# Optimization experiments

Measured on AMD Instinct MI355X. Metric: run time of the kernel, lower is better.

Reference implementation:

```python
import jax, jax.numpy as jnp
import numpy as np

B, S = 8, 2048

def setup_inputs() -> dict:
    key = jax.random.key(0)
    ks = iter(jax.random.split(key, 64))
    def lin(din, dout):
        w = jax.random.normal(next(ks), (din, dout), jnp.float32) / np.float32(np.sqrt(din))
        b = jax.random.normal(next(ks), (dout,), jnp.float32) * 0.01
        return w, b
    inp = {}
    inp['x'] = jax.random.normal(next(ks), (B, S, 256), jnp.float32)
    def blk(tag, d, ff):
        for name, (din, dout) in [('q',(d,d)),('k',(d,d)),('v',(d,d)),('o',(d,d)),('ff1',(d,ff)),('ff2',(ff,d))]:
            w, b = lin(din, dout)
            inp[f'{name}_w{tag}'] = w; inp[f'{name}_b{tag}'] = b
        inp[f'ln1_g{tag}'] = jnp.ones((d,), jnp.float32); inp[f'ln1_b{tag}'] = jnp.zeros((d,), jnp.float32)
        inp[f'ln2_g{tag}'] = jnp.ones((d,), jnp.float32); inp[f'ln2_b{tag}'] = jnp.zeros((d,), jnp.float32)
    blk(1, 256, 1024)
    blk(2, 128, 512)
    for nm, (din, dout) in [('dr1',(256,128)),('dr2',(128,64)),('dr3',(64,32)),('dr4',(32,14))]:
        w, b = lin(din, dout)
        inp[f'{nm}_w'] = w; inp[f'{nm}_b'] = b
    return inp

def _ln(x, g, b, eps=1e-5):
    m = x.mean(-1, keepdims=True)
    v = ((x - m) ** 2).mean(-1, keepdims=True)
    return (x - m) / jnp.sqrt(v + eps) * g + b

def _mha(x, wq, bq, wk, bk, wv, bv, wo, bo, h):
    Bx, Sx, D = x.shape
    hd = D // h
    q = (x @ wq + bq).reshape(Bx, Sx, h, hd).transpose(0, 2, 1, 3)
    k = (x @ wk + bk).reshape(Bx, Sx, h, hd).transpose(0, 2, 1, 3)
    v = (x @ wv + bv).reshape(Bx, Sx, h, hd).transpose(0, 2, 1, 3)
    scores = jnp.einsum('bhqd,bhkd->bhqk', q, k) / jnp.sqrt(jnp.float32(hd))  # [B,h,S,S]
    p = jax.nn.softmax(scores, axis=-1)
    o = jnp.einsum('bhqk,bhkd->bqhd', p, v).reshape(Bx, Sx, D)
    return o @ wo + bo

def _encoder(x, p, h):
    a = _mha(x, p['qw'], p['qb'], p['kw'], p['kb'], p['vw'], p['vb'], p['ow'], p['ob'], h)
    x = _ln(a + x, p['g1'], p['b1'])
    f = jax.nn.relu(x @ p['fw1'] + p['fb1']) @ p['fw2'] + p['fb2']
    return _ln(f + x, p['g2'], p['b2'])

def _pe(s, d):
    pos = jnp.arange(s, dtype=jnp.float32)[:, None]
    dep = jnp.arange(d, dtype=jnp.float32)[None, :]
    ang = pos / jnp.power(jnp.float32(10000.0), dep / d)
    even = (jnp.arange(d)[None, :] % 2) == 0
    return jnp.where(even, jnp.sin(ang), jnp.cos(ang))

def _forward(x,
             q_w1, q_b1, k_w1, k_b1, v_w1, v_b1, o_w1, o_b1,
             ff1_w1, ff1_b1, ff2_w1, ff2_b1, ln1_g1, ln1_b1, ln2_g1, ln2_b1,
             dr1_w, dr1_b,
             q_w2, q_b2, k_w2, k_b2, v_w2, v_b2, o_w2, o_b2,
             ff1_w2, ff1_b2, ff2_w2, ff2_b2, ln1_g2, ln1_b2, ln2_g2, ln2_b2,
             dr2_w, dr2_b, dr3_w, dr3_b, dr4_w, dr4_b):
    h = x + _pe(x.shape[1], x.shape[2])
    p1 = dict(qw=q_w1, qb=q_b1, kw=k_w1, kb=k_b1, vw=v_w1, vb=v_b1, ow=o_w1, ob=o_b1,
              fw1=ff1_w1, fb1=ff1_b1, fw2=ff2_w1, fb2=ff2_b1, g1=ln1_g1, b1=ln1_b1, g2=ln2_g1, b2=ln2_b1)
    h = _encoder(h, p1, 8)
    h = h @ dr1_w + dr1_b
    p2 = dict(qw=q_w2, qb=q_b2, kw=k_w2, kb=k_b2, vw=v_w2, vb=v_b2, ow=o_w2, ob=o_b2,
              fw1=ff1_w2, fb1=ff1_b2, fw2=ff2_w2, fb2=ff2_b2, g1=ln1_g2, b1=ln1_b2, g2=ln2_g2, b2=ln2_b2)
    h = _encoder(h, p2, 8)
    h = h @ dr2_w + dr2_b
    h = jnp.max(h, axis=1)  # AdaptiveMaxPool1d(1) over the sequence dim -> [B, 64]
    h = h @ dr3_w + dr3_b
    return h @ dr4_w + dr4_b  # [B, 14]

def reference(x,
              q_w1, q_b1, k_w1, k_b1, v_w1, v_b1, o_w1, o_b1,
              ff1_w1, ff1_b1, ff2_w1, ff2_b1, ln1_g1, ln1_b1, ln2_g1, ln2_b1,
              dr1_w, dr1_b,
              q_w2, q_b2, k_w2, k_b2, v_w2, v_b2, o_w2, o_b2,
              ff1_w2, ff1_b2, ff2_w2, ff2_b2, ln1_g2, ln1_b2, ln2_g2, ln2_b2,
              dr2_w, dr2_b, dr3_w, dr3_b, dr4_w, dr4_b):
    return _forward(x,
                    q_w1, q_b1, k_w1, k_b1, v_w1, v_b1, o_w1, o_b1,
                    ff1_w1, ff1_b1, ff2_w1, ff2_b1, ln1_g1, ln1_b1, ln2_g1, ln2_b1,
                    dr1_w, dr1_b,
                    q_w2, q_b2, k_w2, k_b2, v_w2, v_b2, o_w2, o_b2,
                    ff1_w2, ff1_b2, ff2_w2, ff2_b2, ln1_g2, ln1_b2, ln2_g2, ln2_b2,
                    dr2_w, dr2_b, dr3_w, dr3_b, dr4_w, dr4_b)
```

## Files before the change

kernel.cpp:

```cpp
#include <hip/hip_runtime.h>
#include <hip/hip_bf16.h>
#include <math.h>

#define SEQ  2048
#define BATCH 8
#define NTOK (SEQ*BATCH)

typedef __attribute__((ext_vector_type(8))) short short8v;
typedef __attribute__((ext_vector_type(4))) float f32x4;
typedef unsigned short u16;

__device__ __forceinline__ u16 f2bf(float f) {
    __hip_bfloat16 h = __float2bfloat16(f);
    return *reinterpret_cast<u16*>(&h);
}
__device__ __forceinline__ float bf2f(u16 u) {
    unsigned v = ((unsigned)u) << 16;
    return *reinterpret_cast<float*>(&v);
}
__device__ __forceinline__ unsigned pack_bf2(float a, float b) {
    __hip_bfloat162 h = __float22bfloat162_rn(float2{a, b});
    return *reinterpret_cast<unsigned*>(&h);
}
__device__ __forceinline__ void gl_lds16(const u16* g, u16* l) {
    __builtin_amdgcn_global_load_lds(
        (const __attribute__((address_space(1))) unsigned int*)g,
        (__attribute__((address_space(3))) unsigned int*)l, 16, 0, 0);
}

struct WDescs {
    const float* src[14];
    int K[14];
    int N[14];
    long dst[14];
    float scale[14];
    int tstart[15];
};

__global__ __launch_bounds__(256) void convert_w_kernel(WDescs d, u16* __restrict__ WA) {
    __shared__ float tile[64][65];
    int blk = blockIdx.x;
    int di = 0;
    while (di < 13 && blk >= d.tstart[di + 1]) ++di;
    int t  = blk - d.tstart[di];
    int K  = d.K[di], N = d.N[di];
    int tn = N >> 6;
    int k0 = (t / tn) << 6, n0 = (t % tn) << 6;
    const float* src = d.src[di];
    float sc = d.scale[di];
    int tid = threadIdx.x;
    #pragma unroll
    for (int i = 0; i < 16; ++i) {
        int id = i * 256 + tid;
        int kk = id >> 6, nn = id & 63;
        tile[kk][nn] = src[(size_t)(k0 + kk) * N + n0 + nn];
    }
    __syncthreads();
    u16* dst = WA + d.dst[di];
    #pragma unroll
    for (int i = 0; i < 16; ++i) {
        int id = i * 256 + tid;
        int nn = id >> 6, kk = id & 63;
        dst[(size_t)(n0 + nn) * K + k0 + kk] = f2bf(tile[kk][nn] * sc);
    }
}

__global__ __launch_bounds__(256) void convert_bias_kernel(
    const float* qb1, const float* kb1, const float* vb1,
    const float* qb2, const float* kb2, const float* vb2,
    const float* dr2b, float* __restrict__ BA, float qs1, float qs2)
{
    int t = blockIdx.x * 256 + threadIdx.x;
    if      (t < 256)  BA[t] = qb1[t] * qs1;
    else if (t < 512)  BA[t] = kb1[t - 256];
    else if (t < 768)  BA[t] = vb1[t - 512];
    else if (t < 896)  BA[t] = qb2[t - 768] * qs2;
    else if (t < 1024) BA[t] = kb2[t - 896];
    else if (t < 1152) BA[t] = vb2[t - 1024];
    else if (t < 1216) BA[t] = dr2b[t - 1152];
    else if (t < 1280) BA[t] = 0.f;
}

__global__ __launch_bounds__(256) void add_pe_kernel(const float* __restrict__ x,
                                                     float* __restrict__ h,
                                                     u16* __restrict__ hb) {
    int idx = blockIdx.x * 256 + threadIdx.x;
    int s = idx >> 8;
    int d = idx & 255;
    float inv = exp2f((float)d * -0.0519051264732f);
    float ang = (float)s * inv;
    float pe  = (d & 1) ? __cosf(ang) : __sinf(ang);
    #pragma unroll
    for (int b = 0; b < BATCH; ++b) {
        size_t g = ((size_t)(b * SEQ + s) << 8) + d;
        float v = x[g] + pe;
        h[g]  = v;
        hb[g] = f2bf(v);
    }
}

template<int BN, int RELU, int WF32, int WBF16, int MAXEP>
__global__ __launch_bounds__(256) void gemm_bf16_kernel(
    const u16* __restrict__ A, const u16* __restrict__ Bt,
    const float* __restrict__ bias, float* __restrict__ Cf,
    u16* __restrict__ Cb, float* __restrict__ Pm, int N, int K)
{
    constexpr int BM  = 64;
    constexpr int NMF = 2;
    constexpr int NBF = BN / 32;
    __shared__ u16 As[2][BM * 64];
    __shared__ u16 Bs[2][BN * 64];
    const int tid  = threadIdx.x;
    const int lane = tid & 63;
    const int c    = lane & 15, g = lane >> 4;
    const int w    = tid >> 6;
    const int wr   = w >> 1, wc = w & 1;
    const size_t bm = (size_t)blockIdx.y * BM;
    const size_t bn = (size_t)blockIdx.x * BN;

    f32x4 acc[NMF][NBF];
    #pragma unroll
    for (int i = 0; i < NMF; ++i)
        #pragma unroll
        for (int j = 0; j < NBF; ++j) acc[i][j] = (f32x4){0.f, 0.f, 0.f, 0.f};

    auto stage = [&](int buf, int t) {
        #pragma unroll
        for (int j = 0; j < BM / 32; ++j) {
            int cid = j * 256 + tid;
            int row = cid >> 3, blk = cid & 7;
            int sof = (blk ^ (row & 7)) * 8;
            gl_lds16(&A[(bm + row) * K + t * 64 + sof], &As[buf][cid * 8]);
        }
        #pragma unroll
        for (int j = 0; j < BN / 32; ++j) {
            int cid = j * 256 + tid;
            int row = cid >> 3, blk = cid & 7;
            int sof = (blk ^ (row & 7)) * 8;
            gl_lds16(&Bt[(bn + row) * K + t * 64 + sof], &Bs[buf][cid * 8]);
        }
    };

    const int nt = K >> 6;
    stage(0, 0);
    __syncthreads();
    for (int t = 0; t < nt; ++t) {
        if (t + 1 < nt) stage((t + 1) & 1, t + 1);
        const int bfi = t & 1;
        #pragma unroll
        for (int ks2 = 0; ks2 < 2; ++ks2) {
            short8v af[NMF], bfr[NBF];
            #pragma unroll
            for (int am = 0; am < NMF; ++am) {
                int r = wr * 32 + am * 16 + c;
                af[am] = *(const short8v*)&As[bfi][r * 64 + (((ks2 * 4 + g) ^ (r & 7)) * 8)];
            }
            #pragma unroll
            for (int bn_ = 0; bn_ < NBF; ++bn_) {
                int r = wc * (BN / 2) + bn_ * 16 + c;
                bfr[bn_] = *(const short8v*)&Bs[bfi][r * 64 + (((ks2 * 4 + g) ^ (r & 7)) * 8)];
            }
            #pragma unroll
            for (int am = 0; am < NMF; ++am)
                #pragma unroll
                for (int bn_ = 0; bn_ < NBF; ++bn_)
                    acc[am][bn_] = __builtin_amdgcn_mfma_f32_16x16x32_bf16(
                                       af[am], bfr[bn_], acc[am][bn_], 0, 0, 0);
        }
        __syncthreads();
    }

    float bv[NBF];
    #pragma unroll
    for (int bn_ = 0; bn_ < NBF; ++bn_) bv[bn_] = bias[bn + wc * (BN / 2) + bn_ * 16 + c];

    if (MAXEP) {
        __shared__ float cm[8][64];
        #pragma unroll
        for (int bn_ = 0; bn_ < NBF; ++bn_) {
            float lm = -INFINITY;
            #pragma unroll
            for (int am = 0; am < NMF; ++am)
                #pragma unroll
                for (int i = 0; i < 4; ++i)
                    lm = fmaxf(lm, acc[am][bn_][i] + bv[bn_]);
            cm[wr * 4 + g][wc * (BN / 2) + bn_ * 16 + c] = lm;
        }
        __syncthreads();
        if (tid < 64) {
            float m = cm[0][tid];
            #pragma unroll
            for (int k = 1; k < 8; ++k) m = fmaxf(m, cm[k][tid]);
            Pm[(size_t)blockIdx.y * 64 + tid] = m;
        }
        return;
    }

    #pragma unroll
    for (int am = 0; am < NMF; ++am) {
        #pragma unroll
        for (int bn_ = 0; bn_ < NBF; ++bn_) {
            #pragma unroll
            for (int i = 0; i < 4; ++i) {
                size_t row = bm + wr * 32 + am * 16 + 4 * g + i;
                size_t col = bn + wc * (BN / 2) + bn_ * 16 + c;
                float v = acc[am][bn_][i] + bv[bn_];
                if (RELU) v = fmaxf(v, 0.f);
                if (WF32)  Cf[row * N + col] = v;
                if (WBF16) Cb[row * N + col] = f2bf(v);
            }
        }
    }
}

template<int D, int WRF>
__global__ __launch_bounds__(256) void ln_residual_kernel(
    const u16* __restrict__ a, const float* __restrict__ r,
    const float* __restrict__ g, const float* __restrict__ bb,
    float* __restrict__ out, u16* __restrict__ outb)
{
    const int N = D >> 6;
    int wave = threadIdx.x >> 6;
    int lane = threadIdx.x & 63;
    size_t token = (size_t)blockIdx.x * 4 + wave;
    const u16*   ar = a + token * D;
    const float* rr = r + token * D;

    float xv[N];
    float s = 0.f;
    #pragma unroll
    for (int i = 0; i < N; ++i) {
        int d = lane + (i << 6);
        xv[i] = bf2f(ar[d]) + rr[d];
        s += xv[i];
    }
    #pragma unroll
    for (int off = 1; off < 64; off <<= 1) s += __shfl_xor(s, off);
    float mean = s * (1.0f / D);
    float vs = 0.f;
    #pragma unroll
    for (int i = 0; i < N; ++i) { float d0 = xv[i] - mean; vs += d0 * d0; }
    #pragma unroll
    for (int off = 1; off < 64; off <<= 1) vs += __shfl_xor(vs, off);
    float inv = 1.0f / sqrtf(vs * (1.0f / D) + 1e-5f);
    #pragma unroll
    for (int i = 0; i < N; ++i) {
        int d = lane + (i << 6);
        float v = (xv[i] - mean) * inv * g[d] + bb[d];
        if (WRF) out[token * D + d] = v;
        outb[token * D + d] = f2bf(v);
    }
}

template<int HD>
__global__ __launch_bounds__(512) void flash_mfma_kernel(
    const u16* __restrict__ QKV, u16* __restrict__ Og, const u16* __restrict__ zsrc)
{
    constexpr int D   = 8 * HD;
    constexpr int SD  = 3 * D;
    constexpr int NDH = HD / 16;

    __shared__ u16 Ks[2][64 * 32];
    __shared__ u16 Vt[2][NDH * 16 * 64];
    __shared__ u16 Pb[128 * 64];

    const int tid  = threadIdx.x;
    const int w    = tid >> 6;
    const int lane = tid & 63;
    const int c    = lane & 15;
    const int g    = lane >> 4;

    const int H    = blockIdx.x + (blockIdx.y << 4);
    const int bh   = H & 63;
    const int qblk = H >> 6;
    const int b = bh >> 3, hh = bh & 7;
    const size_t qvbase = (size_t)b * SEQ * SD + (size_t)hh * HD;
    const size_t obase  = (size_t)b * SEQ * D  + (size_t)hh * HD;
    const int qbase = qblk * 128;

    short8v qf;
    if (HD == 16 && g >= 2) {
        short8v z = {0, 0, 0, 0, 0, 0, 0, 0};
        qf = z;
    } else {
        int qrow = qbase + w * 16 + c;
        qf = *(const short8v*)&QKV[qvbase + (size_t)qrow * SD + 8 * g];
    }

    f32x4 oacc[NDH];
    float lreg[4];
    #pragma unroll
    for (int dh = 0; dh < NDH; ++dh) oacc[dh] = (f32x4){0.f, 0.f, 0.f, 0.f};
    #pragma unroll
    for (int i = 0; i < 4; ++i) lreg[i] = 0.f;

    const bool kstager = (tid < 256);
    const int krow = tid >> 2;
    const int klb  = (tid & 3) ^ ((krow >> 1) & 3);
    const bool kzero = (HD == 16) && (klb >= 2);

    const int vtid = tid - 256;
    const int skey = vtid >> 2;
    const int sch  = (vtid & 3) * 8;
    const bool vstager = (tid >= 256) && (HD == 32 || sch < 16);
    const int spos  = ((skey >> 5) << 5) + 2 * (skey & 15) + ((skey >> 4) & 1);
    const int squad = spos >> 3, soff = spos & 7;
    const int vkc = (c & 7) ^ ((c & 8) >> 1);

    if (kstager)
        gl_lds16(kzero ? zsrc : &QKV[qvbase + (size_t)krow * SD + D + klb * 8],
                 &Ks[0][tid * 8]);
    if (vstager) {
        short8v v0 = *(const short8v*)&QKV[qvbase + (size_t)skey * SD + 2 * D + sch];
        #pragma unroll
        for (int i = 0; i < 8; ++i) {
            int row = sch + i;
            int vk = (row & 7) ^ ((row & 8) >> 1);
            Vt[0][row * 64 + ((squad ^ vk) << 3) + soff] = (u16)v0[i];
        }
    }
    __syncthreads();

    const int NT = SEQ / 64;

    auto tile_body = [&](const int buf, const int t) {
        short8v vv = {0, 0, 0, 0, 0, 0, 0, 0};
        const bool pre = (t + 1 < NT);
        if (pre) {
            if (kstager)
                gl_lds16(kzero ? zsrc
                               : &QKV[qvbase + (size_t)((t + 1) * 64 + krow) * SD + D + klb * 8],
                         &Ks[buf ^ 1][tid * 8]);
            if (vstager)
                vv = *(const short8v*)&QKV[qvbase + (size_t)((t + 1) * 64 + skey) * SD + 2 * D + sch];
        }

        short8v kf[4];
        #pragma unroll
        for (int kh = 0; kh < 4; ++kh) {
            int row = 16 * kh + c;
            kf[kh] = *(const short8v*)&Ks[buf][row * 32 + ((g ^ ((c >> 1) & 3)) * 8)];
        }
        short8v vfr[NDH][2];
        #pragma unroll
        for (int dh = 0; dh < NDH; ++dh) {
            vfr[dh][0] = *(const short8v*)&Vt[buf][(16 * dh + c) * 64 + ((g ^ vkc) << 3)];
            vfr[dh][1] = *(const short8v*)&Vt[buf][(16 * dh + c) * 64 + (((4 + g) ^ vkc) << 3)];
        }

        f32x4 s[4];
        __builtin_amdgcn_s_setprio(1);
        #pragma unroll
        for (int kh = 0; kh < 4; ++kh)
            s[kh] = __builtin_amdgcn_mfma_f32_16x16x32_bf16(
                        qf, kf[kh], (f32x4){0.f, 0.f, 0.f, 0.f}, 0, 0, 0);
        __builtin_amdgcn_s_setprio(0);

        #pragma unroll
        for (int i = 0; i < 4; ++i) {
            float p0 = exp2f(s[0][i]);
            float p1 = exp2f(s[1][i]);
            float p2 = exp2f(s[2][i]);
            float p3 = exp2f(s[3][i]);
            lreg[i] += (p0 + p1) + (p2 + p3);
            int rr = 4 * g + i;
            int pk = (rr & 7) ^ ((rr & 8) >> 1);
            int base = (w * 16 + rr) * 64 + 2 * (c & 3);
            *(unsigned*)&Pb[base + (((c >> 2) ^ pk) << 3)]       = pack_bf2(p0, p1);
            *(unsigned*)&Pb[base + ((((c >> 2) + 4) ^ pk) << 3)] = pack_bf2(p2, p3);
        }

        short8v pf0 = *(const short8v*)&Pb[(w * 16 + c) * 64 + ((g ^ vkc) << 3)];
        short8v pf1 = *(const short8v*)&Pb[(w * 16 + c) * 64 + (((4 + g) ^ vkc) << 3)];
        __builtin_amdgcn_s_setprio(1);
        #pragma unroll
        for (int dh = 0; dh < NDH; ++dh) {
            oacc[dh] = __builtin_amdgcn_mfma_f32_16x16x32_bf16(pf0, vfr[dh][0], oacc[dh], 0, 0, 0);
            oacc[dh] = __builtin_amdgcn_mfma_f32_16x16x32_bf16(pf1, vfr[dh][1], oacc[dh], 0, 0, 0);
        }
        __builtin_amdgcn_s_setprio(0);

        if (pre && vstager) {
            #pragma unroll
            for (int i = 0; i < 8; ++i) {
                int row = sch + i;
                int vk = (row & 7) ^ ((row & 8) >> 1);
                Vt[buf ^ 1][row * 64 + ((squad ^ vk) << 3) + soff] = (u16)vv[i];
            }
        }
        __syncthreads();
    };

    for (int t = 0; t < NT; t += 2) {
        tile_body(0, t);
        tile_body(1, t + 1);
    }

    #pragma unroll
    for (int i = 0; i < 4; ++i) {
        float li = lreg[i];
        li += __shfl_xor(li, 1);
        li += __shfl_xor(li, 2);
        li += __shfl_xor(li, 4);
        li += __shfl_xor(li, 8);
        float inv = 1.0f / li;
        int qrow = qbase + w * 16 + 4 * g + i;
        #pragma unroll
        for (int dh = 0; dh < NDH; ++dh)
            Og[obase + (size_t)qrow * D + 16 * dh + c] = f2bf(oacc[dh][i] * inv);
    }
}

__global__ __launch_bounds__(256) void head_kernel(
    const float* __restrict__ Pm,
    const float* __restrict__ w3, const float* __restrict__ b3,
    const float* __restrict__ w4, const float* __restrict__ b4,
    float* __restrict__ out)
{
    __shared__ float pooled[8][64];
    __shared__ float t2[8][32];
    int tid = threadIdx.x;
    #pragma unroll
    for (int rep = 0; rep < 2; ++rep) {
        int idx = rep * 256 + tid;
        int b = idx >> 6, d = idx & 63;
        float m = -INFINITY;
        #pragma unroll
        for (int k = 0; k < 32; ++k)
            m = fmaxf(m, Pm[(size_t)(b * 32 + k) * 64 + d]);
        pooled[b][d] = m;
    }
    __syncthreads();
    {
        int b = tid >> 5, j = tid & 31;
        float s = b3[j];
        #pragma unroll
        for (int k = 0; k < 64; ++k) s = fmaf(pooled[b][k], w3[k * 32 + j], s);
        t2[b][j] = s;
    }
    __syncthreads();
    if (tid < 8 * 14) {
        int b = tid / 14, j = tid % 14;
        float s = b4[j];
        #pragma unroll
        for (int k = 0; k < 32; ++k) s = fmaf(t2[b][k], w4[k * 14 + j], s);
        out[b * 14 + j] = s;
    }
}

extern "C" void kernel_launch(void* const* d_in, const int* in_sizes, int n_in,
                              void* d_out, int out_size, void* d_ws, size_t ws_size,
                              hipStream_t stream) {
    const float* x     = (const float*)d_in[0];
    const float* qw1   = (const float*)d_in[1];
    const float* qb1   = (const float*)d_in[2];
    const float* kw1   = (const float*)d_in[3];
    const float* kb1   = (const float*)d_in[4];
    const float* vw1   = (const float*)d_in[5];
    const float* vb1   = (const float*)d_in[6];
    const float* ow1   = (const float*)d_in[7];
    const float* ob1   = (const float*)d_in[8];
    const float* f1w1  = (const float*)d_in[9];
    const float* f1b1  = (const float*)d_in[10];
    const float* f2w1  = (const float*)d_in[11];
    const float* f2b1  = (const float*)d_in[12];
    const float* ln1g1 = (const float*)d_in[13];
    const float* ln1b1 = (const float*)d_in[14];
    const float* ln2g1 = (const float*)d_in[15];
    const float* ln2b1 = (const float*)d_in[16];
    const float* qw2   = (const float*)d_in[17];
    const float* qb2   = (const float*)d_in[18];
    const float* kw2   = (const float*)d_in[19];
    const float* kb2   = (const float*)d_in[20];
    const float* vw2   = (const float*)d_in[21];
    const float* vb2   = (const float*)d_in[22];
    const float* ow2   = (const float*)d_in[23];
    const float* ob2   = (const float*)d_in[24];
    const float* f1w2  = (const float*)d_in[25];
    const float* f1b2  = (const float*)d_in[26];
    const float* f2w2  = (const float*)d_in[27];
    const float* f2b2  = (const float*)d_in[28];
    const float* ln1g2 = (const float*)d_in[29];
    const float* ln1b2 = (const float*)d_in[30];
    const float* ln2g2 = (const float*)d_in[31];
    const float* ln2b2 = (const float*)d_in[32];
    const float* dr1w  = (const float*)d_in[33];
    const float* dr1b  = (const float*)d_in[34];
    const float* dr2w  = (const float*)d_in[35];
    const float* dr2b  = (const float*)d_in[36];
    const float* dr3w  = (const float*)d_in[37];
    const float* dr3b  = (const float*)d_in[38];
    const float* dr4w  = (const float*)d_in[39];
    const float* dr4b  = (const float*)d_in[40];

    const size_t T = NTOK;
    float* F1 = (float*)d_ws;
    float* F2 = F1 + T * 256;
    u16*   E1 = (u16*)(F2 + T * 256);
    u16*   E2 = E1 + T * 256;
    u16*   E3 = E2 + T * 256;
    u16*   Dq = E3 + T * 256;
    u16*   WA = Dq + T * 1024;
    float* BA = (float*)(WA + 1048576);
    const u16* ZS = (const u16*)(BA + 1216);

    const float QS1 = 0.25503488f;
    const float QS2 = 0.36067376f;

    WDescs wd;
    const float* srcs[14] = {qw1, kw1, vw1, ow1, f1w1, f2w1, dr1w,
                             qw2, kw2, vw2, ow2, f1w2, f2w2, dr2w};
    int Ks_[14]  = {256, 256, 256, 256, 256, 1024, 256, 128, 128, 128, 128, 128, 512, 128};
    int Ns_[14]  = {256, 256, 256, 256, 1024, 256, 128, 128, 128, 128, 128, 512, 128, 64};
    long dsts[14] = {0, 65536, 131072, 196608, 262144, 524288, 786432,
                     819200, 835584, 851968, 868352, 884736, 950272, 1015808};
    float scs[14] = {QS1, 1.f, 1.f, 1.f, 1.f, 1.f, 1.f, QS2, 1.f, 1.f, 1.f, 1.f, 1.f, 1.f};
    int tst[15] = {0, 16, 32, 48, 64, 128, 192, 200, 204, 208, 212, 216, 232, 248, 250};
    for (int i = 0; i < 14; ++i) {
        wd.src[i] = srcs[i]; wd.K[i] = Ks_[i]; wd.N[i] = Ns_[i];
        wd.dst[i] = dsts[i]; wd.scale[i] = scs[i];
    }
    for (int i = 0; i < 15; ++i) wd.tstart[i] = tst[i];

    const dim3 blk(256);
    const dim3 blk512(512);

    convert_w_kernel<<<250, blk, 0, stream>>>(wd, WA);
    convert_bias_kernel<<<5, blk, 0, stream>>>(qb1, kb1, vb1, qb2, kb2, vb2, dr2b, BA, QS1, QS2);

    add_pe_kernel<<<SEQ, blk, 0, stream>>>(x, F1, E1);

    gemm_bf16_kernel<128,0,0,1,0><<<dim3(6, 256), blk, 0, stream>>>(E1, WA + 0,      BA,   nullptr, Dq, nullptr, 768, 256);
    flash_mfma_kernel<32><<<dim3(16, 64), blk512, 0, stream>>>(Dq, E2, ZS);
    gemm_bf16_kernel< 64,0,0,1,0><<<dim3(4, 256), blk, 0, stream>>>(E2, WA + 196608, ob1,  nullptr, E3, nullptr, 256, 256);
    ln_residual_kernel<256,1><<<NTOK / 4, blk, 0, stream>>>(E3, F1, ln1g1, ln1b1, F1, E1);
    gemm_bf16_kernel<128,1,0,1,0><<<dim3(8, 256), blk, 0, stream>>>(E1, WA + 262144, f1b1, nullptr, Dq, nullptr, 1024, 256);
    gemm_bf16_kernel< 64,0,0,1,0><<<dim3(4, 256), blk, 0, stream>>>(Dq, WA + 524288, f2b1, nullptr, E3, nullptr, 256, 1024);
    ln_residual_kernel<256,1><<<NTOK / 4, blk, 0, stream>>>(E3, F1, ln2g1, ln2b1, F1, E1);

    gemm_bf16_kernel< 64,0,1,1,0><<<dim3(2, 256), blk, 0, stream>>>(E1, WA + 786432, dr1b, F2, E2, nullptr, 128, 256);

    gemm_bf16_kernel<128,0,0,1,0><<<dim3(3, 256), blk, 0, stream>>>(E2, WA + 819200, BA + 768, nullptr, Dq, nullptr, 384, 128);
    flash_mfma_kernel<16><<<dim3(16, 64), blk512, 0, stream>>>(Dq, E3, ZS);
    gemm_bf16_kernel< 64,0,0,1,0><<<dim3(2, 256), blk, 0, stream>>>(E3, WA + 868352, ob2,  nullptr, E2, nullptr, 128, 128);
    ln_residual_kernel<128,1><<<NTOK / 4, blk, 0, stream>>>(E2, F2, ln1g2, ln1b2, F2, E1);
    gemm_bf16_kernel<128,1,0,1,0><<<dim3(4, 256), blk, 0, stream>>>(E1, WA + 884736, f1b2, nullptr, Dq, nullptr, 512, 128);
    gemm_bf16_kernel< 64,0,0,1,0><<<dim3(2, 256), blk, 0, stream>>>(Dq, WA + 950272, f2b2, nullptr, E2, nullptr, 128, 512);
    ln_residual_kernel<128,0><<<NTOK / 4, blk, 0, stream>>>(E2, F2, ln2g2, ln2b2, nullptr, E1);

    gemm_bf16_kernel< 64,0,0,0,1><<<dim3(1, 256), blk, 0, stream>>>(E1, WA + 1015808, BA + 1152, nullptr, nullptr, F1, 64, 128);
    head_kernel<<<1, blk, 0, stream>>>(F1, dr3w, dr3b, dr4w, dr4b, (float*)d_out);
}
```

Baseline: 489.9 us.

## Merge bias conversion into weight-conversion kernel and drop MFMA priority hints

The bias-packing kernel is folded into the weight-conversion kernel as six extra blocks, which removes one kernel launch. Separately, the s_setprio raise and lower calls around the MFMA sections of the flash attention kernel are removed, leaving the wave scheduler's default priority. The merge saves a small launch cost, while dropping the priority hints changes how waves interleave and could help or hurt attention throughput.

```diff
diff --git a/kernel.cpp b/kernel.cpp
--- a/kernel.cpp
+++ b/kernel.cpp
@@ -35,11 +35,29 @@
     long dst[14];
     float scale[14];
     int tstart[15];
+    const float* qb1; const float* kb1; const float* vb1;
+    const float* qb2; const float* kb2; const float* vb2;
+    const float* dr2b;
+    float qs1, qs2;
 };
 
-__global__ __launch_bounds__(256) void convert_w_kernel(WDescs d, u16* __restrict__ WA) {
+__global__ __launch_bounds__(256) void convert_w_kernel(WDescs d, u16* __restrict__ WA,
+                                                        float* __restrict__ BA) {
+    int blk = blockIdx.x;
+    int tid = threadIdx.x;
+    if (blk >= 250) {
+        int t = (blk - 250) * 256 + tid;
+        if      (t < 256)  BA[t] = d.qb1[t] * d.qs1;
+        else if (t < 512)  BA[t] = d.kb1[t - 256];
+        else if (t < 768)  BA[t] = d.vb1[t - 512];
+        else if (t < 896)  BA[t] = d.qb2[t - 768] * d.qs2;
+        else if (t < 1024) BA[t] = d.kb2[t - 896];
+        else if (t < 1152) BA[t] = d.vb2[t - 1024];
+        else if (t < 1216) BA[t] = d.dr2b[t - 1152];
+        else if (t < 1280) BA[t] = 0.f;
+        return;
+    }
     __shared__ float tile[64][65];
-    int blk = blockIdx.x;
     int di = 0;
     while (di < 13 && blk >= d.tstart[di + 1]) ++di;
     int t  = blk - d.tstart[di];
@@ -48,7 +66,6 @@
     int k0 = (t / tn) << 6, n0 = (t % tn) << 6;
     const float* src = d.src[di];
     float sc = d.scale[di];
-    int tid = threadIdx.x;
     #pragma unroll
     for (int i = 0; i < 16; ++i) {
         int id = i * 256 + tid;
@@ -63,22 +80,6 @@
         int nn = id >> 6, kk = id & 63;
         dst[(size_t)(n0 + nn) * K + k0 + kk] = f2bf(tile[kk][nn] * sc);
     }
-}
-
-__global__ __launch_bounds__(256) void convert_bias_kernel(
-    const float* qb1, const float* kb1, const float* vb1,
-    const float* qb2, const float* kb2, const float* vb2,
-    const float* dr2b, float* __restrict__ BA, float qs1, float qs2)
-{
-    int t = blockIdx.x * 256 + threadIdx.x;
-    if      (t < 256)  BA[t] = qb1[t] * qs1;
-    else if (t < 512)  BA[t] = kb1[t - 256];
-    else if (t < 768)  BA[t] = vb1[t - 512];
-    else if (t < 896)  BA[t] = qb2[t - 768] * qs2;
-    else if (t < 1024) BA[t] = kb2[t - 896];
-    else if (t < 1152) BA[t] = vb2[t - 1024];
-    else if (t < 1216) BA[t] = dr2b[t - 1152];
-    else if (t < 1280) BA[t] = 0.f;
 }
 
 __global__ __launch_bounds__(256) void add_pe_kernel(const float* __restrict__ x,
@@ -349,12 +350,10 @@
         }
 
         f32x4 s[4];
-        __builtin_amdgcn_s_setprio(1);
         #pragma unroll
         for (int kh = 0; kh < 4; ++kh)
             s[kh] = __builtin_amdgcn_mfma_f32_16x16x32_bf16(
                         qf, kf[kh], (f32x4){0.f, 0.f, 0.f, 0.f}, 0, 0, 0);
-        __builtin_amdgcn_s_setprio(0);
 
         #pragma unroll
         for (int i = 0; i < 4; ++i) {
@@ -372,13 +371,11 @@
 
         short8v pf0 = *(const short8v*)&Pb[(w * 16 + c) * 64 + ((g ^ vkc) << 3)];
         short8v pf1 = *(const short8v*)&Pb[(w * 16 + c) * 64 + (((4 + g) ^ vkc) << 3)];
-        __builtin_amdgcn_s_setprio(1);
         #pragma unroll
         for (int dh = 0; dh < NDH; ++dh) {
             oacc[dh] = __builtin_amdgcn_mfma_f32_16x16x32_bf16(pf0, vfr[dh][0], oacc[dh], 0, 0, 0);
             oacc[dh] = __builtin_amdgcn_mfma_f32_16x16x32_bf16(pf1, vfr[dh][1], oacc[dh], 0, 0, 0);
         }
-        __builtin_amdgcn_s_setprio(0);
 
         if (pre && vstager) {
             #pragma unroll
@@ -521,12 +518,14 @@
         wd.dst[i] = dsts[i]; wd.scale[i] = scs[i];
     }
     for (int i = 0; i < 15; ++i) wd.tstart[i] = tst[i];
+    wd.qb1 = qb1; wd.kb1 = kb1; wd.vb1 = vb1;
+    wd.qb2 = qb2; wd.kb2 = kb2; wd.vb2 = vb2;
+    wd.dr2b = dr2b; wd.qs1 = QS1; wd.qs2 = QS2;
 
     const dim3 blk(256);
     const dim3 blk512(512);
 
-    convert_w_kernel<<<250, blk, 0, stream>>>(wd, WA);
-    convert_bias_kernel<<<5, blk, 0, stream>>>(qb1, kb1, vb1, qb2, kb2, vb2, dr2b, BA, QS1, QS2);
+    convert_w_kernel<<<256, blk, 0, stream>>>(wd, WA, BA);
 
     add_pe_kernel<<<SEQ, blk, 0, stream>>>(x, F1, E1);
 
```

After: 483.8 us. No clear change (-1.3%).
